# Optimization experiments

Measured on AMD Instinct MI355X. Metric: run time of the kernel, lower is better.

The kernel has to match this reference:

```python
import jax, jax.numpy as jnp
import numpy as np

EMBED = 256
HEADS = 8
LEVELS = 4
POINTS = 4
HD = EMBED // HEADS  # 32
SHAPES = np.array([[100, 100], [50, 50], [25, 25], [13, 13]], dtype=np.int64)  # (H_l, W_l)


def setup_inputs() -> dict:
    key = jax.random.key(0)
    ks = jax.random.split(key, 12)
    nv = int(SHAPES.prod(-1).sum())  # 13294
    bs, nq, d = 2, nv, EMBED
    level_start = np.concatenate([[0], SHAPES.prod(-1).cumsum()[:-1]])
    s = 0.02
    return {
        "query": jax.random.normal(ks[0], (bs, nq, d), jnp.float32),
        "reference_points": jax.random.uniform(ks[1], (bs, nq, LEVELS, 2), jnp.float32),
        "value": jax.random.normal(ks[2], (bs, nv, d), jnp.float32),
        "spatial_shapes": jnp.asarray(SHAPES, jnp.int32),
        "level_start_index": jnp.asarray(level_start, jnp.int32),
        "key_padding_mask": jnp.zeros((bs, nv), jnp.bool_),
        "W_samp": jax.random.normal(ks[3], (HEADS * LEVELS * POINTS * 2, d), jnp.float32) * s,
        "b_samp": jax.random.normal(ks[4], (HEADS * LEVELS * POINTS * 2,), jnp.float32),
        "W_attn": jax.random.normal(ks[5], (HEADS * LEVELS * POINTS, d), jnp.float32) * s,
        "b_attn": jnp.zeros((HEADS * LEVELS * POINTS,), jnp.float32),
        "W_val": jax.random.normal(ks[6], (d, d), jnp.float32) * s,
        "b_val": jnp.zeros((d,), jnp.float32),
        "W_out": jax.random.normal(ks[7], (d, d), jnp.float32) * s,
        "b_out": jnp.zeros((d,), jnp.float32),
    }


def _msda_core(value_bhnd, shapes_np, starts_np, loc, attn):
    """value_bhnd: (bs, H, nv, hd); loc: (bs, nq, H, L, P, 2) in [0,1]; attn: (bs, nq, H, L, P)."""
    bs, heads, nv, hd = value_bhnd.shape
    nq = loc.shape[1]
    out = jnp.zeros((bs, nq, heads, hd), value_bhnd.dtype)
    for l in range(LEVELS):
        H, W = int(shapes_np[l, 0]), int(shapes_np[l, 1])
        start = int(starts_np[l])
        v = jax.lax.dynamic_slice_in_dim(value_bhnd, start, H * W, axis=2)  # (bs, heads, H*W, hd)
        # grid_sample(align_corners=False): pixel coord = loc * size - 0.5
        lx = loc[:, :, :, l, :, 0] * W - 0.5  # (bs, nq, heads, P)
        ly = loc[:, :, :, l, :, 1] * H - 0.5
        x0 = jnp.floor(lx)
        y0 = jnp.floor(ly)
        tx = lx - x0
        ty = ly - y0
        x0i = x0.astype(jnp.int32)
        y0i = y0.astype(jnp.int32)
        samp = jnp.zeros((bs, heads, nq, POINTS, hd), value_bhnd.dtype)
        for dy, wy in ((0, 1.0 - ty), (1, ty)):
            for dx, wx in ((0, 1.0 - tx), (1, tx)):
                xi = x0i + dx
                yi = y0i + dy
                valid = (xi >= 0) & (xi < W) & (yi >= 0) & (yi < H)  # zeros padding
                idx = jnp.clip(yi, 0, H - 1) * W + jnp.clip(xi, 0, W - 1)  # (bs, nq, heads, P)
                idx_t = idx.transpose(0, 2, 1, 3).reshape(bs, heads, nq * POINTS)
                g = jnp.take_along_axis(v, idx_t[..., None], axis=2)
                g = g.reshape(bs, heads, nq, POINTS, hd)
                w = jnp.where(valid, wx * wy, 0.0).transpose(0, 2, 1, 3)[..., None]
                samp = samp + g * w
        out = out + jnp.einsum("bhqpd,bqhp->bqhd", samp, attn[:, :, :, l, :])
    return out.reshape(bs, nq, heads * hd)


def reference(query, reference_points, value, spatial_shapes, level_start_index,
              key_padding_mask, W_samp, b_samp, W_attn, b_attn, W_val, b_val, W_out, b_out):
    bs, nq, d = query.shape
    v = value @ W_val.T + b_val
    v = jnp.where(key_padding_mask[..., None], 0.0, v)
    v = v.reshape(bs, -1, HEADS, HD).transpose(0, 2, 1, 3)  # (bs, heads, nv, hd)
    off = (query @ W_samp.T + b_samp).reshape(bs, nq, HEADS, LEVELS, POINTS, 2)
    attn = (query @ W_attn.T + b_attn).reshape(bs, nq, HEADS, LEVELS * POINTS)
    attn = jax.nn.softmax(attn, axis=-1).reshape(bs, nq, HEADS, LEVELS, POINTS)
    ss = np.asarray(spatial_shapes)
    starts = np.asarray(level_start_index)
    # offset normalizer is (W, H) per level
    norm = jnp.asarray(ss[:, ::-1].copy(), jnp.float32)
    loc = reference_points[:, :, None, :, None, :] + off / norm[None, None, None, :, None, :]
    out = _msda_core(v, ss, starts, loc, attn)
    return out @ W_out.T + b_out
```

## Files before the change

kernel.cpp:

```cpp
#include <hip/hip_runtime.h>
#include <hip/hip_bf16.h>
#include <hip/hip_fp16.h>
#include <cstdint>
#include <cstddef>

#define EMBED  256
#define NV_PER_B 13294
#define M_PAD   26624
#define QCH    16

__constant__ const int c_H[4]  = {100, 50, 25, 13};
__constant__ const int c_W[4]  = {100, 50, 25, 13};
__constant__ const int c_ST[4] = {0, 10000, 12500, 13125};

typedef __attribute__((ext_vector_type(8))) short bf16x8;
typedef __attribute__((ext_vector_type(4))) float f32x4;

__device__ inline short f2bf(float x) {
    __hip_bfloat16 h = __float2bfloat16(x);
    return *reinterpret_cast<short*>(&h);
}

__device__ __forceinline__ void fmamix_lo(float& acc, unsigned w16, unsigned v2) {
    asm("v_fma_mix_f32 %0, %1, %2, %0 op_sel:[0,0,0] op_sel_hi:[1,1,0]"
        : "+v"(acc) : "v"(w16), "v"(v2));
}
__device__ __forceinline__ void fmamix_hi(float& acc, unsigned w16, unsigned v2) {
    asm("v_fma_mix_f32 %0, %1, %2, %0 op_sel:[0,1,0] op_sel_hi:[1,1,0]"
        : "+v"(acc) : "v"(w16), "v"(v2));
}

__global__ __launch_bounds__(256) void convert_kernel(
    const float* __restrict__ q,  const float* __restrict__ v,
    const float* __restrict__ wv, const float* __restrict__ wsamp,
    const float* __restrict__ wattn, const float* __restrict__ wo,
    const float* __restrict__ bsamp, const float* __restrict__ battn,
    short* __restrict__ q_bf, short* __restrict__ v_bf,
    short* __restrict__ wv_bf, short* __restrict__ wcat_bf,
    short* __restrict__ wo_bf, float* __restrict__ bias_cat,
    int n_real4, int n_pad4)
{
    const int i = blockIdx.x * 256 + threadIdx.x;
    if (i < n_pad4) {
        float4 a = make_float4(0.f, 0.f, 0.f, 0.f);
        float4 b = make_float4(0.f, 0.f, 0.f, 0.f);
        if (i < n_real4) {
            a = ((const float4*)q)[i];
            b = ((const float4*)v)[i];
        }
        ((short4*)q_bf)[i] = make_short4(f2bf(a.x), f2bf(a.y), f2bf(a.z), f2bf(a.w));
        ((short4*)v_bf)[i] = make_short4(f2bf(b.x), f2bf(b.y), f2bf(b.z), f2bf(b.w));
    }
    if (i < 16384) {
        float4 a = ((const float4*)wv)[i];
        float4 c = ((const float4*)wo)[i];
        ((short4*)wv_bf)[i] = make_short4(f2bf(a.x), f2bf(a.y), f2bf(a.z), f2bf(a.w));
        ((short4*)wo_bf)[i] = make_short4(f2bf(c.x), f2bf(c.y), f2bf(c.z), f2bf(c.w));
    }
    if (i < 24576) {
        float4 a = (i < 16384) ? ((const float4*)wsamp)[i]
                               : ((const float4*)wattn)[i - 16384];
        ((short4*)wcat_bf)[i] = make_short4(f2bf(a.x), f2bf(a.y), f2bf(a.z), f2bf(a.w));
    }
    if (i < 96) {
        float4 a = (i < 64) ? ((const float4*)bsamp)[i]
                            : ((const float4*)battn)[i - 64];
        ((float4*)bias_cat)[i] = a;
    }
}

__device__ __forceinline__ void gemm_kloop(
    const short* __restrict__ A, const short* __restrict__ Wt,
    int bm, int bn, char* smem, f32x4 (&acc)[4][4],
    int t, int wave, int lane)
{
    constexpr int K = 256;
    const int row0 = t >> 2, row1 = row0 + 64;
    const int kbl  = t & 3;
    const int kbg0 = kbl ^ (row0 & 3);
    const int kbg1 = kbl ^ (row1 & 3);
    const size_t a0 = (size_t)(bm + row0) * K + kbg0 * 8;
    const size_t a1 = (size_t)(bm + row1) * K + kbg1 * 8;
    const size_t b0 = (size_t)(bn + row0) * K + kbg0 * 8;
    const size_t b1 = (size_t)(bn + row1) * K + kbg1 * 8;
    const int lr16 = lane & 15, qk = lane >> 4;
    const int swz  = (qk ^ (lr16 & 3)) * 16;
    const int wrow = wave & 1, wcol = wave >> 1;

    auto issue = [&](int stage, int k0) {
        char* sa = smem + stage * 16384 + wave * 1024;
        char* sb = sa + 8192;
        __builtin_amdgcn_global_load_lds(
            (const __attribute__((address_space(1))) void*)(A + a0 + k0),
            (__attribute__((address_space(3))) void*)(sa), 16, 0, 0);
        __builtin_amdgcn_global_load_lds(
            (const __attribute__((address_space(1))) void*)(A + a1 + k0),
            (__attribute__((address_space(3))) void*)(sa + 4096), 16, 0, 0);
        __builtin_amdgcn_global_load_lds(
            (const __attribute__((address_space(1))) void*)(Wt + b0 + k0),
            (__attribute__((address_space(3))) void*)(sb), 16, 0, 0);
        __builtin_amdgcn_global_load_lds(
            (const __attribute__((address_space(1))) void*)(Wt + b1 + k0),
            (__attribute__((address_space(3))) void*)(sb + 4096), 16, 0, 0);
    };

    issue(0, 0);
    #pragma unroll
    for (int it = 0; it < 8; ++it) {
        __syncthreads();
        if (it + 1 < 8) issue((it + 1) & 1, (it + 1) * 32);
        const char* sa = smem + (it & 1) * 16384;
        const char* sb = sa + 8192;
        bf16x8 af[4], bfr[4];
        #pragma unroll
        for (int mi = 0; mi < 4; ++mi)
            af[mi] = *(const bf16x8*)(sa + (wrow * 64 + mi * 16 + lr16) * 64 + swz);
        #pragma unroll
        for (int ni = 0; ni < 4; ++ni)
            bfr[ni] = *(const bf16x8*)(sb + (wcol * 64 + ni * 16 + lr16) * 64 + swz);
        #pragma unroll
        for (int mi = 0; mi < 4; ++mi)
            #pragma unroll
            for (int ni = 0; ni < 4; ++ni)
                acc[mi][ni] = __builtin_amdgcn_mfma_f32_16x16x32_bf16(
                    af[mi], bfr[ni], acc[mi][ni], 0, 0, 0);
    }
}

__global__ __launch_bounds__(256) void gemm_mega_kernel(
    const short* __restrict__ v_bf, const short* __restrict__ wv_bf,
    const float* __restrict__ b_val, __half* __restrict__ vproj,
    const short* __restrict__ q_bf, const short* __restrict__ wcat_bf,
    const float* __restrict__ bias_cat, __half* __restrict__ qo)
{
    __shared__ __align__(16) char smem[36864];
    const int t = threadIdx.x;
    const int wave = t >> 6, lane = t & 63;
    const int lr16 = lane & 15, qk = lane >> 4;
    const int wrow = wave & 1, wcol = wave >> 1;
    const int y = blockIdx.y;
    const int bm = blockIdx.x * 128;

    const short* A; const short* Wt; const float* bias; __half* Cc; int Nst, bn;
    if (y < 2) { A = v_bf; Wt = wv_bf;   bias = b_val;    Cc = vproj; Nst = 256; bn = y * 128; }
    else       { A = q_bf; Wt = wcat_bf; bias = bias_cat; Cc = qo;    Nst = 384; bn = (y - 2) * 128; }

    f32x4 acc[4][4] = {};
    gemm_kloop(A, Wt, bm, bn, smem, acc, t, wave, lane);

    __syncthreads();
    __half* ep = (__half*)(smem + wave * 9216);
    const int colbase = bn + wcol * 64;
    float bv[4];
    #pragma unroll
    for (int ni = 0; ni < 4; ++ni) bv[ni] = bias[colbase + ni * 16 + lr16];
    #pragma unroll
    for (int mi = 0; mi < 4; ++mi)
        #pragma unroll
        for (int ni = 0; ni < 4; ++ni)
            #pragma unroll
            for (int r = 0; r < 4; ++r)
                ep[(mi * 16 + qk * 4 + r) * 72 + ni * 16 + lr16] =
                    __float2half(acc[mi][ni][r] + bv[ni]);
    __syncthreads();
    const int er = lane >> 3, ec = (lane & 7) * 8;
    #pragma unroll
    for (int pass = 0; pass < 8; ++pass) {
        const int r = pass * 8 + er;
        const int4 vv = *(const int4*)&ep[r * 72 + ec];
        const int grow = bm + wrow * 64 + r;
        if (y < 2) {
            if (grow < 2 * NV_PER_B) {
                const int bb  = (grow >= NV_PER_B) ? 1 : 0;
                const int ii  = grow - bb * NV_PER_B;
                const int col = colbase + ec;
                const size_t dst =
                    ((size_t)(bb * 8 + (col >> 5)) * NV_PER_B + ii) * 32 + (col & 31);
                *(int4*)&Cc[dst] = vv;
            }
        } else {
            *(int4*)&Cc[(size_t)grow * Nst + colbase + ec] = vv;
        }
    }
}

__global__ __launch_bounds__(256) void gemm_out_kernel(
    const short* __restrict__ corebf, const short* __restrict__ wo_bf,
    const float* __restrict__ b_out, float* __restrict__ C, int M)
{
    __shared__ __align__(16) char smem[36864];
    const int t = threadIdx.x;
    const int wave = t >> 6, lane = t & 63;
    const int lr16 = lane & 15, qk = lane >> 4;
    const int wrow = wave & 1, wcol = wave >> 1;
    const int bm = blockIdx.x * 128, bn = blockIdx.y * 128;

    f32x4 acc[4][4] = {};
    gemm_kloop(corebf, wo_bf, bm, bn, smem, acc, t, wave, lane);

    const int colbase = bn + wcol * 64;
    float bv[4];
    #pragma unroll
    for (int ni = 0; ni < 4; ++ni) bv[ni] = b_out[colbase + ni * 16 + lr16];
    float* ep = (float*)(smem + wave * 8704);
    #pragma unroll
    for (int p = 0; p < 2; ++p) {
        __syncthreads();
        #pragma unroll
        for (int mh = 0; mh < 2; ++mh) {
            const int mi = p * 2 + mh;
            #pragma unroll
            for (int ni = 0; ni < 4; ++ni)
                #pragma unroll
                for (int r = 0; r < 4; ++r)
                    ep[(mh * 16 + qk * 4 + r) * 68 + ni * 16 + lr16] =
                        acc[mi][ni][r] + bv[ni];
        }
        __syncthreads();
        const int er = lane >> 4, ec = (lane & 15) * 4;
        #pragma unroll
        for (int j = 0; j < 8; ++j) {
            const int r = j * 4 + er;
            const float4 vv = *(const float4*)&ep[r * 68 + ec];
            const int grow = bm + wrow * 64 + p * 32 + r;
            if (grow < M)
                *(float4*)&C[(size_t)grow * 256 + colbase + ec] = vv;
        }
    }
}

__global__ __launch_bounds__(256) void msda_core_kernel(
    const __half* __restrict__ vproj,
    const float* __restrict__ refp,
    const __half* __restrict__ qo,
    short* __restrict__ core,
    int nq, int nv, int M)
{
    const int t = threadIdx.x;
    const int head  = blockIdx.x & 7;
    const int chunk = blockIdx.x >> 3;
    const int q  = t >> 4;
    const int gq = chunk * QCH + q;

    __shared__ __align__(16) uint2 s_tap[QCH][2][2][18];

    {
        const int lp = t & 15, l = lp >> 2;
        const int gqc = min(gq, M - 1);
        const float logit = __half2float(qo[(size_t)gq * 384 + 256 + head * 16 + lp]);
        float m = logit;
        #pragma unroll
        for (int s = 1; s < 16; s <<= 1) m = fmaxf(m, __shfl_xor(m, s));
        const float ev = expf(logit - m);
        float ssum = ev;
        #pragma unroll
        for (int s = 1; s < 16; s <<= 1) ssum += __shfl_xor(ssum, s);
        const float aw = ev / ssum;

        const float2 off = __half22float2(
            *(const __half2*)&qo[(size_t)gq * 384 + (head * 16 + lp) * 2]);
        const float rx = refp[(size_t)gqc * 8 + l * 2];
        const float ry = refp[(size_t)gqc * 8 + l * 2 + 1];
        const int W = c_W[l], H = c_H[l], st = c_ST[l];
        const float fW = (float)W, fH = (float)H;
        const float lx = (rx + off.x / fW) * fW - 0.5f;
        const float ly = (ry + off.y / fH) * fH - 0.5f;
        const float x0f = floorf(lx), y0f = floorf(ly);
        const float fx = lx - x0f, fy = ly - y0f;
        const int x0 = (int)x0f, y0 = (int)y0f;
        const int x0c = min(max(x0, 0), W - 2);
        const float wx0 = (x0c == x0) ? (1.f - fx) : ((x0c == x0 + 1) ? fx : 0.f);
        const float wx1 = (x0c + 1 == x0) ? (1.f - fx) : ((x0c == x0) ? fx : 0.f);
        const int b = (gq >= nq) ? 1 : 0;
        const unsigned plane = (unsigned)((b * 8 + head) * nv);
        #pragma unroll
        for (int dy = 0; dy < 2; ++dy) {
            const int yv = y0 + dy;
            const bool okY = (yv >= 0) & (yv < H);
            const int yc = min(max(yv, 0), H - 1);
            const float wy = okY ? (dy ? fy : (1.f - fy)) * aw : 0.f;
            const unsigned boff = (plane + (unsigned)(st + yc * W + x0c)) << 6;
            s_tap[q][dy][0][lp] = make_uint2(
                boff, (unsigned)__half_as_ushort(__float2half(wy * wx0)));
            s_tap[q][dy][1][lp] = make_uint2(
                boff + 64u, (unsigned)__half_as_ushort(__float2half(wy * wx1)));
        }
    }
    __syncthreads();

    const int g   = t & 15;
    const int y   = g >> 3;
    const int xh  = (g >> 2) & 1;
    const int c8  = g & 3;
    const char* __restrict__ vbase = (const char*)vproj + c8 * 16;

    const uint2* taps = &s_tap[q][y][xh][0];
    float a[8] = {0.f, 0.f, 0.f, 0.f, 0.f, 0.f, 0.f, 0.f};
    #pragma unroll
    for (int p = 0; p < 16; p += 2) {
        const uint4 d = *(const uint4*)&taps[p];
        const int4 r0 = *(const int4*)(vbase + (size_t)d.x);
        const int4 r1 = *(const int4*)(vbase + (size_t)d.z);
        const unsigned* u0 = (const unsigned*)&r0;
        const unsigned* u1 = (const unsigned*)&r1;
        fmamix_lo(a[0], d.y, u0[0]); fmamix_hi(a[1], d.y, u0[0]);
        fmamix_lo(a[2], d.y, u0[1]); fmamix_hi(a[3], d.y, u0[1]);
        fmamix_lo(a[4], d.y, u0[2]); fmamix_hi(a[5], d.y, u0[2]);
        fmamix_lo(a[6], d.y, u0[3]); fmamix_hi(a[7], d.y, u0[3]);
        fmamix_lo(a[0], d.w, u1[0]); fmamix_hi(a[1], d.w, u1[0]);
        fmamix_lo(a[2], d.w, u1[1]); fmamix_hi(a[3], d.w, u1[1]);
        fmamix_lo(a[4], d.w, u1[2]); fmamix_hi(a[5], d.w, u1[2]);
        fmamix_lo(a[6], d.w, u1[3]); fmamix_hi(a[7], d.w, u1[3]);
    }
    #pragma unroll
    for (int i = 0; i < 8; ++i) a[i] += __shfl_xor(a[i], 4);
    #pragma unroll
    for (int i = 0; i < 8; ++i) a[i] += __shfl_xor(a[i], 8);

    if (((g & 12) == 0) && gq < M) {
        __align__(16) short o[8];
        #pragma unroll
        for (int i = 0; i < 8; ++i) o[i] = f2bf(a[i]);
        *(int4*)&core[(size_t)gq * 256 + head * 32 + c8 * 8] = *(const int4*)o;
    }
}

extern "C" void kernel_launch(void* const* d_in, const int* in_sizes, int n_in,
                              void* d_out, int out_size, void* d_ws, size_t ws_size,
                              hipStream_t stream) {
    const float* query  = (const float*)d_in[0];
    const float* refp   = (const float*)d_in[1];
    const float* value  = (const float*)d_in[2];
    const float* W_samp = (const float*)d_in[6];
    const float* b_samp = (const float*)d_in[7];
    const float* W_attn = (const float*)d_in[8];
    const float* b_attn = (const float*)d_in[9];
    const float* W_val  = (const float*)d_in[10];
    const float* b_val  = (const float*)d_in[11];
    const float* W_out  = (const float*)d_in[12];
    const float* b_out  = (const float*)d_in[13];
    float* out = (float*)d_out;

    const int M  = in_sizes[0] / EMBED;
    const int nq = NV_PER_B;
    const int nv = NV_PER_B;
    const int Mp = M_PAD;

    char* p = (char*)d_ws;
    short*  q_bf   = (short*)p;  p += (size_t)Mp * 256 * 2;
    short*  v_bf   = (short*)p;  p += (size_t)Mp * 256 * 2;
    short*  corebf = (short*)p;  p += (size_t)Mp * 256 * 2;
    __half* vproj  = (__half*)p; p += (size_t)Mp * 256 * 2;
    __half* qo     = (__half*)p; p += (size_t)Mp * 384 * 2;
    short*  wv_bf  = (short*)p;  p += 65536 * 2;
    short*  wcat   = (short*)p;  p += 98304 * 2;
    short*  wo_bf  = (short*)p;  p += 65536 * 2;
    float*  biascat= (float*)p;  p += 384 * 4;

    const int n_real4 = M * 256 / 4;
    const int n_pad4  = Mp * 256 / 4;
    dim3 blk(256);

    convert_kernel<<<dim3((n_pad4 + 255) / 256), blk, 0, stream>>>(
        query, value, W_val, W_samp, W_attn, W_out, b_samp, b_attn,
        q_bf, v_bf, wv_bf, wcat, wo_bf, biascat, n_real4, n_pad4);

    const int mb = Mp / 128;
    gemm_mega_kernel<<<dim3(mb, 5), blk, 0, stream>>>(
        v_bf, wv_bf, b_val, vproj, q_bf, wcat, biascat, qo);

    const int nchunks = (M + QCH - 1) / QCH;
    msda_core_kernel<<<dim3(8 * nchunks), blk, 0, stream>>>(
        vproj, refp, qo, corebf, nq, nv, M);

    gemm_out_kernel<<<dim3(mb, 2), blk, 0, stream>>>(
        corebf, wo_bf, b_out, out, M);
}
```

Before: 189.3 us.

## Fuse fp32-to-bf16 conversion into GEMM loaders and remap blocks per XCD

Removes the separate convert kernel. The GEMMs now load fp32 activations and weights directly, convert them to bf16 in registers and store them to LDS, with register prefetch of the next K slice. Grid indexing is also remapped so that consecutive M tiles land on the same XCD, which should improve L2 reuse. This saves a full pass that wrote bf16 copies and one kernel launch, but doubles global read bytes inside the GEMM and replaces async global-to-LDS loads with register staging.

```diff
diff --git a/kernel.cpp b/kernel.cpp
--- a/kernel.cpp
+++ b/kernel.cpp
@@ -21,6 +21,13 @@
     return *reinterpret_cast<short*>(&h);
 }
 
+__device__ __forceinline__ bf16x8 cvt8(const float4& x, const float4& y) {
+    bf16x8 o;
+    o[0] = f2bf(x.x); o[1] = f2bf(x.y); o[2] = f2bf(x.z); o[3] = f2bf(x.w);
+    o[4] = f2bf(y.x); o[5] = f2bf(y.y); o[6] = f2bf(y.z); o[7] = f2bf(y.w);
+    return o;
+}
+
 __device__ __forceinline__ void fmamix_lo(float& acc, unsigned w16, unsigned v2) {
     asm("v_fma_mix_f32 %0, %1, %2, %0 op_sel:[0,0,0] op_sel_hi:[1,1,0]"
         : "+v"(acc) : "v"(w16), "v"(v2));
@@ -30,85 +37,117 @@
         : "+v"(acc) : "v"(w16), "v"(v2));
 }
 
-__global__ __launch_bounds__(256) void convert_kernel(
-    const float* __restrict__ q,  const float* __restrict__ v,
-    const float* __restrict__ wv, const float* __restrict__ wsamp,
-    const float* __restrict__ wattn, const float* __restrict__ wo,
-    const float* __restrict__ bsamp, const float* __restrict__ battn,
-    short* __restrict__ q_bf, short* __restrict__ v_bf,
-    short* __restrict__ wv_bf, short* __restrict__ wcat_bf,
-    short* __restrict__ wo_bf, float* __restrict__ bias_cat,
-    int n_real4, int n_pad4)
-{
-    const int i = blockIdx.x * 256 + threadIdx.x;
-    if (i < n_pad4) {
-        float4 a = make_float4(0.f, 0.f, 0.f, 0.f);
-        float4 b = make_float4(0.f, 0.f, 0.f, 0.f);
-        if (i < n_real4) {
-            a = ((const float4*)q)[i];
-            b = ((const float4*)v)[i];
-        }
-        ((short4*)q_bf)[i] = make_short4(f2bf(a.x), f2bf(a.y), f2bf(a.z), f2bf(a.w));
-        ((short4*)v_bf)[i] = make_short4(f2bf(b.x), f2bf(b.y), f2bf(b.z), f2bf(b.w));
-    }
-    if (i < 16384) {
-        float4 a = ((const float4*)wv)[i];
-        float4 c = ((const float4*)wo)[i];
-        ((short4*)wv_bf)[i] = make_short4(f2bf(a.x), f2bf(a.y), f2bf(a.z), f2bf(a.w));
-        ((short4*)wo_bf)[i] = make_short4(f2bf(c.x), f2bf(c.y), f2bf(c.z), f2bf(c.w));
-    }
-    if (i < 24576) {
-        float4 a = (i < 16384) ? ((const float4*)wsamp)[i]
-                               : ((const float4*)wattn)[i - 16384];
-        ((short4*)wcat_bf)[i] = make_short4(f2bf(a.x), f2bf(a.y), f2bf(a.z), f2bf(a.w));
-    }
-    if (i < 96) {
-        float4 a = (i < 64) ? ((const float4*)bsamp)[i]
-                            : ((const float4*)battn)[i - 64];
-        ((float4*)bias_cat)[i] = a;
-    }
-}
-
-__device__ __forceinline__ void gemm_kloop(
-    const short* __restrict__ A, const short* __restrict__ Wt,
-    int bm, int bn, char* smem, f32x4 (&acc)[4][4],
+__device__ __forceinline__ void gemm_kloop_f32f32(
+    const float* __restrict__ A, const float* __restrict__ B,
+    int bm, int M, char* smem, f32x4 (&acc)[4][4],
     int t, int wave, int lane)
 {
-    constexpr int K = 256;
     const int row0 = t >> 2, row1 = row0 + 64;
     const int kbl  = t & 3;
     const int kbg0 = kbl ^ (row0 & 3);
     const int kbg1 = kbl ^ (row1 & 3);
-    const size_t a0 = (size_t)(bm + row0) * K + kbg0 * 8;
-    const size_t a1 = (size_t)(bm + row1) * K + kbg1 * 8;
-    const size_t b0 = (size_t)(bn + row0) * K + kbg0 * 8;
-    const size_t b1 = (size_t)(bn + row1) * K + kbg1 * 8;
+    const float* pa0 = A + (size_t)(bm + row0) * 256 + kbg0 * 8;
+    const float* pa1 = A + (size_t)(bm + row1) * 256 + kbg1 * 8;
+    const float* pb0 = B + (size_t)row0 * 256 + kbg0 * 8;
+    const float* pb1 = B + (size_t)row1 * 256 + kbg1 * 8;
+    const bool va0 = (bm + row0) < M;
+    const bool va1 = (bm + row1) < M;
     const int lr16 = lane & 15, qk = lane >> 4;
     const int swz  = (qk ^ (lr16 & 3)) * 16;
     const int wrow = wave & 1, wcol = wave >> 1;
-
-    auto issue = [&](int stage, int k0) {
+    const int slot = wave * 1024 + lane * 16;
+
+    float4 r[8];
+    auto ld = [&](int k0) {
+        const float4 z = make_float4(0.f, 0.f, 0.f, 0.f);
+        r[0] = va0 ? *(const float4*)(pa0 + k0)     : z;
+        r[1] = va0 ? *(const float4*)(pa0 + k0 + 4) : z;
+        r[2] = va1 ? *(const float4*)(pa1 + k0)     : z;
+        r[3] = va1 ? *(const float4*)(pa1 + k0 + 4) : z;
+        r[4] = *(const float4*)(pb0 + k0);
+        r[5] = *(const float4*)(pb0 + k0 + 4);
+        r[6] = *(const float4*)(pb1 + k0);
+        r[7] = *(const float4*)(pb1 + k0 + 4);
+    };
+    auto st = [&](int stage) {
+        char* base = smem + stage * 16384 + slot;
+        *(bf16x8*)(base)         = cvt8(r[0], r[1]);
+        *(bf16x8*)(base + 4096)  = cvt8(r[2], r[3]);
+        *(bf16x8*)(base + 8192)  = cvt8(r[4], r[5]);
+        *(bf16x8*)(base + 12288) = cvt8(r[6], r[7]);
+    };
+
+    ld(0); st(0);
+    #pragma unroll
+    for (int it = 0; it < 8; ++it) {
+        if (it + 1 < 8) ld((it + 1) * 32);
+        __syncthreads();
+        const char* sa = smem + (it & 1) * 16384;
+        const char* sb = sa + 8192;
+        bf16x8 af[4], bfr[4];
+        #pragma unroll
+        for (int mi = 0; mi < 4; ++mi)
+            af[mi] = *(const bf16x8*)(sa + (wrow * 64 + mi * 16 + lr16) * 64 + swz);
+        #pragma unroll
+        for (int ni = 0; ni < 4; ++ni)
+            bfr[ni] = *(const bf16x8*)(sb + (wcol * 64 + ni * 16 + lr16) * 64 + swz);
+        #pragma unroll
+        for (int mi = 0; mi < 4; ++mi)
+            #pragma unroll
+            for (int ni = 0; ni < 4; ++ni)
+                acc[mi][ni] = __builtin_amdgcn_mfma_f32_16x16x32_bf16(
+                    af[mi], bfr[ni], acc[mi][ni], 0, 0, 0);
+        if (it + 1 < 8) st((it + 1) & 1);
+    }
+}
+
+__device__ __forceinline__ void gemm_kloop_bf_f32(
+    const short* __restrict__ A, const float* __restrict__ B,
+    int bm, char* smem, f32x4 (&acc)[4][4],
+    int t, int wave, int lane)
+{
+    const int row0 = t >> 2, row1 = row0 + 64;
+    const int kbl  = t & 3;
+    const int kbg0 = kbl ^ (row0 & 3);
+    const int kbg1 = kbl ^ (row1 & 3);
+    const size_t a0 = (size_t)(bm + row0) * 256 + kbg0 * 8;
+    const size_t a1 = (size_t)(bm + row1) * 256 + kbg1 * 8;
+    const float* pb0 = B + (size_t)row0 * 256 + kbg0 * 8;
+    const float* pb1 = B + (size_t)row1 * 256 + kbg1 * 8;
+    const int lr16 = lane & 15, qk = lane >> 4;
+    const int swz  = (qk ^ (lr16 & 3)) * 16;
+    const int wrow = wave & 1, wcol = wave >> 1;
+    const int slot = wave * 1024 + lane * 16;
+
+    auto issueA = [&](int stage, int k0) {
         char* sa = smem + stage * 16384 + wave * 1024;
-        char* sb = sa + 8192;
         __builtin_amdgcn_global_load_lds(
             (const __attribute__((address_space(1))) void*)(A + a0 + k0),
             (__attribute__((address_space(3))) void*)(sa), 16, 0, 0);
         __builtin_amdgcn_global_load_lds(
             (const __attribute__((address_space(1))) void*)(A + a1 + k0),
             (__attribute__((address_space(3))) void*)(sa + 4096), 16, 0, 0);
-        __builtin_amdgcn_global_load_lds(
-            (const __attribute__((address_space(1))) void*)(Wt + b0 + k0),
-            (__attribute__((address_space(3))) void*)(sb), 16, 0, 0);
-        __builtin_amdgcn_global_load_lds(
-            (const __attribute__((address_space(1))) void*)(Wt + b1 + k0),
-            (__attribute__((address_space(3))) void*)(sb + 4096), 16, 0, 0);
     };
 
-    issue(0, 0);
+    float4 r[4];
+    auto ldB = [&](int k0) {
+        r[0] = *(const float4*)(pb0 + k0);
+        r[1] = *(const float4*)(pb0 + k0 + 4);
+        r[2] = *(const float4*)(pb1 + k0);
+        r[3] = *(const float4*)(pb1 + k0 + 4);
+    };
+    auto stB = [&](int stage) {
+        char* base = smem + stage * 16384 + slot;
+        *(bf16x8*)(base + 8192)  = cvt8(r[0], r[1]);
+        *(bf16x8*)(base + 12288) = cvt8(r[2], r[3]);
+    };
+
+    issueA(0, 0); ldB(0); stB(0);
     #pragma unroll
     for (int it = 0; it < 8; ++it) {
+        if (it + 1 < 8) ldB((it + 1) * 32);
         __syncthreads();
-        if (it + 1 < 8) issue((it + 1) & 1, (it + 1) * 32);
+        if (it + 1 < 8) issueA((it + 1) & 1, (it + 1) * 32);
         const char* sa = smem + (it & 1) * 16384;
         const char* sb = sa + 8192;
         bf16x8 af[4], bfr[4];
@@ -124,36 +163,47 @@
             for (int ni = 0; ni < 4; ++ni)
                 acc[mi][ni] = __builtin_amdgcn_mfma_f32_16x16x32_bf16(
                     af[mi], bfr[ni], acc[mi][ni], 0, 0, 0);
+        if (it + 1 < 8) stB((it + 1) & 1);
     }
 }
 
 __global__ __launch_bounds__(256) void gemm_mega_kernel(
-    const short* __restrict__ v_bf, const short* __restrict__ wv_bf,
-    const float* __restrict__ b_val, __half* __restrict__ vproj,
-    const short* __restrict__ q_bf, const short* __restrict__ wcat_bf,
-    const float* __restrict__ bias_cat, __half* __restrict__ qo)
+    const float* __restrict__ vf, const float* __restrict__ qf,
+    const float* __restrict__ W_val, const float* __restrict__ W_samp,
+    const float* __restrict__ W_attn,
+    const float* __restrict__ b_val, const float* __restrict__ b_samp,
+    const float* __restrict__ b_attn,
+    __half* __restrict__ vproj, __half* __restrict__ qo, int M)
 {
     __shared__ __align__(16) char smem[36864];
     const int t = threadIdx.x;
     const int wave = t >> 6, lane = t & 63;
     const int lr16 = lane & 15, qk = lane >> 4;
     const int wrow = wave & 1, wcol = wave >> 1;
-    const int y = blockIdx.y;
-    const int bm = blockIdx.x * 128;
-
-    const short* A; const short* Wt; const float* bias; __half* Cc; int Nst, bn;
-    if (y < 2) { A = v_bf; Wt = wv_bf;   bias = b_val;    Cc = vproj; Nst = 256; bn = y * 128; }
-    else       { A = q_bf; Wt = wcat_bf; bias = bias_cat; Cc = qo;    Nst = 384; bn = (y - 2) * 128; }
+
+    const int wg  = blockIdx.x;
+    const int xcd = wg & 7, j = wg >> 3;
+    const int bm  = (xcd * 26 + j / 5) * 128;
+    const int y   = j % 5;
+
+    const float* A; const float* B; int bn;
+    if (y < 2)      { A = vf; B = W_val  + (size_t)y * 128 * 256;       bn = y * 128; }
+    else if (y < 4) { A = qf; B = W_samp + (size_t)(y - 2) * 128 * 256; bn = (y - 2) * 128; }
+    else            { A = qf; B = W_attn;                               bn = 256; }
 
     f32x4 acc[4][4] = {};
-    gemm_kloop(A, Wt, bm, bn, smem, acc, t, wave, lane);
+    gemm_kloop_f32f32(A, B, bm, M, smem, acc, t, wave, lane);
+
+    __half* Cc = (y < 2) ? vproj : qo;
+    const int Nst = (y < 2) ? 256 : 384;
+    const float* bias = (y < 2) ? b_val : ((y == 4) ? b_attn : b_samp);
 
     __syncthreads();
     __half* ep = (__half*)(smem + wave * 9216);
     const int colbase = bn + wcol * 64;
     float bv[4];
     #pragma unroll
-    for (int ni = 0; ni < 4; ++ni) bv[ni] = bias[colbase + ni * 16 + lr16];
+    for (int ni = 0; ni < 4; ++ni) bv[ni] = bias[(colbase + ni * 16 + lr16) & 255];
     #pragma unroll
     for (int mi = 0; mi < 4; ++mi)
         #pragma unroll
@@ -185,7 +235,7 @@
 }
 
 __global__ __launch_bounds__(256) void gemm_out_kernel(
-    const short* __restrict__ corebf, const short* __restrict__ wo_bf,
+    const short* __restrict__ corebf, const float* __restrict__ W_out,
     const float* __restrict__ b_out, float* __restrict__ C, int M)
 {
     __shared__ __align__(16) char smem[36864];
@@ -193,10 +243,14 @@
     const int wave = t >> 6, lane = t & 63;
     const int lr16 = lane & 15, qk = lane >> 4;
     const int wrow = wave & 1, wcol = wave >> 1;
-    const int bm = blockIdx.x * 128, bn = blockIdx.y * 128;
+
+    const int wg  = blockIdx.x;
+    const int xcd = wg & 7, j = wg >> 3;
+    const int bm  = (xcd * 26 + (j >> 1)) * 128;
+    const int bn  = (j & 1) * 128;
 
     f32x4 acc[4][4] = {};
-    gemm_kloop(corebf, wo_bf, bm, bn, smem, acc, t, wave, lane);
+    gemm_kloop_bf_f32(corebf, W_out + (size_t)bn * 256, bm, smem, acc, t, wave, lane);
 
     const int colbase = bn + wcol * 64;
     float bv[4];
@@ -219,8 +273,8 @@
         __syncthreads();
         const int er = lane >> 4, ec = (lane & 15) * 4;
         #pragma unroll
-        for (int j = 0; j < 8; ++j) {
-            const int r = j * 4 + er;
+        for (int j2 = 0; j2 < 8; ++j2) {
+            const int r = j2 * 4 + er;
             const float4 vv = *(const float4*)&ep[r * 68 + ec];
             const int grow = bm + wrow * 64 + p * 32 + r;
             if (grow < M)
@@ -347,32 +401,20 @@
     const int Mp = M_PAD;
 
     char* p = (char*)d_ws;
-    short*  q_bf   = (short*)p;  p += (size_t)Mp * 256 * 2;
-    short*  v_bf   = (short*)p;  p += (size_t)Mp * 256 * 2;
     short*  corebf = (short*)p;  p += (size_t)Mp * 256 * 2;
     __half* vproj  = (__half*)p; p += (size_t)Mp * 256 * 2;
     __half* qo     = (__half*)p; p += (size_t)Mp * 384 * 2;
-    short*  wv_bf  = (short*)p;  p += 65536 * 2;
-    short*  wcat   = (short*)p;  p += 98304 * 2;
-    short*  wo_bf  = (short*)p;  p += 65536 * 2;
-    float*  biascat= (float*)p;  p += 384 * 4;
-
-    const int n_real4 = M * 256 / 4;
-    const int n_pad4  = Mp * 256 / 4;
+
     dim3 blk(256);
 
-    convert_kernel<<<dim3((n_pad4 + 255) / 256), blk, 0, stream>>>(
-        query, value, W_val, W_samp, W_attn, W_out, b_samp, b_attn,
-        q_bf, v_bf, wv_bf, wcat, wo_bf, biascat, n_real4, n_pad4);
-
-    const int mb = Mp / 128;
-    gemm_mega_kernel<<<dim3(mb, 5), blk, 0, stream>>>(
-        v_bf, wv_bf, b_val, vproj, q_bf, wcat, biascat, qo);
+    gemm_mega_kernel<<<dim3(1040), blk, 0, stream>>>(
+        value, query, W_val, W_samp, W_attn, b_val, b_samp, b_attn,
+        vproj, qo, M);
 
     const int nchunks = (M + QCH - 1) / QCH;
     msda_core_kernel<<<dim3(8 * nchunks), blk, 0, stream>>>(
         vproj, refp, qo, corebf, nq, nv, M);
 
-    gemm_out_kernel<<<dim3(mb, 2), blk, 0, stream>>>(
-        corebf, wo_bf, b_out, out, M);
-}
+    gemm_out_kernel<<<dim3(416), blk, 0, stream>>>(
+        corebf, W_out, b_out, out, M);
+}
```

Result: slower. 215.7 us (+13.9%).

## Halve GEMM M-tile to 64 and preload the whole A tile into LDS

Applied to the files above, without the earlier changes.

Both GEMM kernels move from 128x128 to 64x128 output tiles, which doubles the grid so more blocks are spread across the CUs. The full 64x256 A slab is now loaded into LDS up front in eight chunks, while the weight tile stays double-buffered per K-step. This grows LDS use to 48KB per block and halves the MFMA work per wave per K-step. The cost is more redundant weight-tile loads overall and possibly lower occupancy from the larger shared memory footprint.

```diff
diff --git a/kernel.cpp b/kernel.cpp
--- a/kernel.cpp
+++ b/kernel.cpp
@@ -71,31 +71,31 @@
 
 __device__ __forceinline__ void gemm_kloop(
     const short* __restrict__ A, const short* __restrict__ Wt,
-    int bm, int bn, char* smem, f32x4 (&acc)[4][4],
+    int bm, int bn, char* smem, f32x4 (&acc)[2][4],
     int t, int wave, int lane)
 {
     constexpr int K = 256;
-    const int row0 = t >> 2, row1 = row0 + 64;
+    const int row  = t >> 2;
+    const int rowB = row + 64;
     const int kbl  = t & 3;
-    const int kbg0 = kbl ^ (row0 & 3);
-    const int kbg1 = kbl ^ (row1 & 3);
-    const size_t a0 = (size_t)(bm + row0) * K + kbg0 * 8;
-    const size_t a1 = (size_t)(bm + row1) * K + kbg1 * 8;
-    const size_t b0 = (size_t)(bn + row0) * K + kbg0 * 8;
-    const size_t b1 = (size_t)(bn + row1) * K + kbg1 * 8;
+    const int kbgA = kbl ^ (row  & 3);
+    const int kbgB = kbl ^ (rowB & 3);
+    const size_t aoff = (size_t)(bm + row) * K + kbgA * 8;
+    const size_t b0   = (size_t)(bn + row)  * K + kbgA * 8;
+    const size_t b1   = (size_t)(bn + rowB) * K + kbgB * 8;
     const int lr16 = lane & 15, qk = lane >> 4;
     const int swz  = (qk ^ (lr16 & 3)) * 16;
     const int wrow = wave & 1, wcol = wave >> 1;
 
-    auto issue = [&](int stage, int k0) {
-        char* sa = smem + stage * 16384 + wave * 1024;
-        char* sb = sa + 8192;
+    #pragma unroll
+    for (int s = 0; s < 8; ++s) {
+        char* sa = smem + s * 4096 + wave * 1024;
         __builtin_amdgcn_global_load_lds(
-            (const __attribute__((address_space(1))) void*)(A + a0 + k0),
+            (const __attribute__((address_space(1))) void*)(A + aoff + s * 32),
             (__attribute__((address_space(3))) void*)(sa), 16, 0, 0);
-        __builtin_amdgcn_global_load_lds(
-            (const __attribute__((address_space(1))) void*)(A + a1 + k0),
-            (__attribute__((address_space(3))) void*)(sa + 4096), 16, 0, 0);
+    }
+    auto issueB = [&](int st, int k0) {
+        char* sb = smem + 32768 + st * 8192 + wave * 1024;
         __builtin_amdgcn_global_load_lds(
             (const __attribute__((address_space(1))) void*)(Wt + b0 + k0),
             (__attribute__((address_space(3))) void*)(sb), 16, 0, 0);
@@ -103,23 +103,22 @@
             (const __attribute__((address_space(1))) void*)(Wt + b1 + k0),
             (__attribute__((address_space(3))) void*)(sb + 4096), 16, 0, 0);
     };
-
-    issue(0, 0);
+    issueB(0, 0);
     #pragma unroll
     for (int it = 0; it < 8; ++it) {
         __syncthreads();
-        if (it + 1 < 8) issue((it + 1) & 1, (it + 1) * 32);
-        const char* sa = smem + (it & 1) * 16384;
-        const char* sb = sa + 8192;
-        bf16x8 af[4], bfr[4];
-        #pragma unroll
-        for (int mi = 0; mi < 4; ++mi)
-            af[mi] = *(const bf16x8*)(sa + (wrow * 64 + mi * 16 + lr16) * 64 + swz);
+        if (it + 1 < 8) issueB((it + 1) & 1, (it + 1) * 32);
+        const char* sa = smem + it * 4096;
+        const char* sb = smem + 32768 + (it & 1) * 8192;
+        bf16x8 af[2], bfr[4];
+        #pragma unroll
+        for (int mi = 0; mi < 2; ++mi)
+            af[mi] = *(const bf16x8*)(sa + (wrow * 32 + mi * 16 + lr16) * 64 + swz);
         #pragma unroll
         for (int ni = 0; ni < 4; ++ni)
             bfr[ni] = *(const bf16x8*)(sb + (wcol * 64 + ni * 16 + lr16) * 64 + swz);
         #pragma unroll
-        for (int mi = 0; mi < 4; ++mi)
+        for (int mi = 0; mi < 2; ++mi)
             #pragma unroll
             for (int ni = 0; ni < 4; ++ni)
                 acc[mi][ni] = __builtin_amdgcn_mfma_f32_16x16x32_bf16(
@@ -133,29 +132,29 @@
     const short* __restrict__ q_bf, const short* __restrict__ wcat_bf,
     const float* __restrict__ bias_cat, __half* __restrict__ qo)
 {
-    __shared__ __align__(16) char smem[36864];
+    __shared__ __align__(16) char smem[49152];
     const int t = threadIdx.x;
     const int wave = t >> 6, lane = t & 63;
     const int lr16 = lane & 15, qk = lane >> 4;
     const int wrow = wave & 1, wcol = wave >> 1;
     const int y = blockIdx.y;
-    const int bm = blockIdx.x * 128;
+    const int bm = blockIdx.x * 64;
 
     const short* A; const short* Wt; const float* bias; __half* Cc; int Nst, bn;
     if (y < 2) { A = v_bf; Wt = wv_bf;   bias = b_val;    Cc = vproj; Nst = 256; bn = y * 128; }
     else       { A = q_bf; Wt = wcat_bf; bias = bias_cat; Cc = qo;    Nst = 384; bn = (y - 2) * 128; }
 
-    f32x4 acc[4][4] = {};
+    f32x4 acc[2][4] = {};
     gemm_kloop(A, Wt, bm, bn, smem, acc, t, wave, lane);
 
     __syncthreads();
-    __half* ep = (__half*)(smem + wave * 9216);
+    __half* ep = (__half*)(smem + wave * 4608);
     const int colbase = bn + wcol * 64;
     float bv[4];
     #pragma unroll
     for (int ni = 0; ni < 4; ++ni) bv[ni] = bias[colbase + ni * 16 + lr16];
     #pragma unroll
-    for (int mi = 0; mi < 4; ++mi)
+    for (int mi = 0; mi < 2; ++mi)
         #pragma unroll
         for (int ni = 0; ni < 4; ++ni)
             #pragma unroll
@@ -165,10 +164,10 @@
     __syncthreads();
     const int er = lane >> 3, ec = (lane & 7) * 8;
     #pragma unroll
-    for (int pass = 0; pass < 8; ++pass) {
+    for (int pass = 0; pass < 4; ++pass) {
         const int r = pass * 8 + er;
         const int4 vv = *(const int4*)&ep[r * 72 + ec];
-        const int grow = bm + wrow * 64 + r;
+        const int grow = bm + wrow * 32 + r;
         if (y < 2) {
             if (grow < 2 * NV_PER_B) {
                 const int bb  = (grow >= NV_PER_B) ? 1 : 0;
@@ -188,14 +187,14 @@
     const short* __restrict__ corebf, const short* __restrict__ wo_bf,
     const float* __restrict__ b_out, float* __restrict__ C, int M)
 {
-    __shared__ __align__(16) char smem[36864];
+    __shared__ __align__(16) char smem[49152];
     const int t = threadIdx.x;
     const int wave = t >> 6, lane = t & 63;
     const int lr16 = lane & 15, qk = lane >> 4;
     const int wrow = wave & 1, wcol = wave >> 1;
-    const int bm = blockIdx.x * 128, bn = blockIdx.y * 128;
-
-    f32x4 acc[4][4] = {};
+    const int bm = blockIdx.x * 64, bn = blockIdx.y * 128;
+
+    f32x4 acc[2][4] = {};
     gemm_kloop(corebf, wo_bf, bm, bn, smem, acc, t, wave, lane);
 
     const int colbase = bn + wcol * 64;
@@ -203,29 +202,24 @@
     #pragma unroll
     for (int ni = 0; ni < 4; ++ni) bv[ni] = b_out[colbase + ni * 16 + lr16];
     float* ep = (float*)(smem + wave * 8704);
-    #pragma unroll
-    for (int p = 0; p < 2; ++p) {
-        __syncthreads();
-        #pragma unroll
-        for (int mh = 0; mh < 2; ++mh) {
-            const int mi = p * 2 + mh;
+    __syncthreads();
+    #pragma unroll
+    for (int mi = 0; mi < 2; ++mi)
+        #pragma unroll
+        for (int ni = 0; ni < 4; ++ni)
             #pragma unroll
-            for (int ni = 0; ni < 4; ++ni)
-                #pragma unroll
-                for (int r = 0; r < 4; ++r)
-                    ep[(mh * 16 + qk * 4 + r) * 68 + ni * 16 + lr16] =
-                        acc[mi][ni][r] + bv[ni];
-        }
-        __syncthreads();
-        const int er = lane >> 4, ec = (lane & 15) * 4;
-        #pragma unroll
-        for (int j = 0; j < 8; ++j) {
-            const int r = j * 4 + er;
-            const float4 vv = *(const float4*)&ep[r * 68 + ec];
-            const int grow = bm + wrow * 64 + p * 32 + r;
-            if (grow < M)
-                *(float4*)&C[(size_t)grow * 256 + colbase + ec] = vv;
-        }
+            for (int r = 0; r < 4; ++r)
+                ep[(mi * 16 + qk * 4 + r) * 68 + ni * 16 + lr16] =
+                    acc[mi][ni][r] + bv[ni];
+    __syncthreads();
+    const int er = lane >> 4, ec = (lane & 15) * 4;
+    #pragma unroll
+    for (int j = 0; j < 8; ++j) {
+        const int r = j * 4 + er;
+        const float4 vv = *(const float4*)&ep[r * 68 + ec];
+        const int grow = bm + wrow * 32 + r;
+        if (grow < M)
+            *(float4*)&C[(size_t)grow * 256 + colbase + ec] = vv;
     }
 }
 
@@ -365,7 +359,7 @@
         query, value, W_val, W_samp, W_attn, W_out, b_samp, b_attn,
         q_bf, v_bf, wv_bf, wcat, wo_bf, biascat, n_real4, n_pad4);
 
-    const int mb = Mp / 128;
+    const int mb = Mp / 64;
     gemm_mega_kernel<<<dim3(mb, 5), blk, 0, stream>>>(
         v_bf, wv_bf, b_val, vproj, q_bf, wcat, biascat, qo);
 
```

Result: no change. 188.7 us (-0.3%).
